# Kernel tuning notes

Hardware: AMD Instinct MI355X
Metric: run time of the kernel (lower is better)

The kernel has to match this reference:

```python
import jax, jax.numpy as jnp
import numpy as np

D_MODEL = 1024
N_LAYERS = 2
D_INNER = 2048   # expand_factor * d_model
D_STATE = 16
DT_RANK = 64     # ceil(d_model/16)
D_CONV = 4
BATCH = 2
SEQ = 1024
EPS = 1e-5


def setup_inputs() -> dict:
    key = jax.random.key(0)
    ks = jax.random.split(key, 8)
    s = 0.02
    x = jax.random.normal(ks[0], (BATCH, SEQ, D_MODEL), jnp.float32)
    norm_w = jnp.ones((N_LAYERS, D_MODEL), jnp.float32)
    in_proj_w = jax.random.normal(ks[1], (N_LAYERS, 2 * D_INNER, D_MODEL), jnp.float32) * s
    conv_w = jax.random.normal(ks[2], (N_LAYERS, D_INNER, D_CONV), jnp.float32) * s  # depthwise kernel
    conv_b = jnp.zeros((N_LAYERS, D_INNER), jnp.float32)
    x_proj_w = jax.random.normal(ks[3], (N_LAYERS, DT_RANK + 2 * D_STATE, D_INNER), jnp.float32) * s
    dt_std = DT_RANK ** -0.5
    dt_proj_w = jax.random.uniform(ks[4], (N_LAYERS, D_INNER, DT_RANK), jnp.float32, -dt_std, dt_std)
    dt = jnp.exp(jax.random.uniform(ks[5], (N_LAYERS, D_INNER), jnp.float32)
                 * (np.log(0.1) - np.log(0.001)) + np.log(0.001))
    dt = jnp.clip(dt, 1e-4)
    dt_proj_b = dt + jnp.log(-jnp.expm1(-dt))  # inverse softplus init
    A_log = jnp.broadcast_to(jnp.log(jnp.arange(1, D_STATE + 1, dtype=jnp.float32)),
                             (N_LAYERS, D_INNER, D_STATE)).copy()
    D_param = jnp.ones((N_LAYERS, D_INNER), jnp.float32)
    out_proj_w = jax.random.normal(ks[6], (N_LAYERS, D_MODEL, D_INNER), jnp.float32) * s
    return dict(x=x, norm_w=norm_w, in_proj_w=in_proj_w, conv_w=conv_w, conv_b=conv_b,
                x_proj_w=x_proj_w, dt_proj_w=dt_proj_w, dt_proj_b=dt_proj_b,
                A_log=A_log, D_param=D_param, out_proj_w=out_proj_w)


def _rms_norm(x, w):
    return x * jax.lax.rsqrt(jnp.mean(x * x, axis=-1, keepdims=True) + EPS) * w


def _silu(x):
    return x * jax.nn.sigmoid(x)


def _mamba_block(x, in_w, cw, cb, xp_w, dt_w, dt_b, A_log, Dp, out_w):
    # x: (B, L, D)
    xz = x @ in_w.T                      # (B, L, 2*ED)
    xc, z = jnp.split(xz, 2, axis=-1)    # each (B, L, ED)
    # causal depthwise conv1d (torch pads d_conv-1 both sides then slices [:L])
    xpad = jnp.pad(xc, ((0, 0), (D_CONV - 1, 0), (0, 0)))
    L = xc.shape[1]
    xc = sum(xpad[:, k:k + L, :] * cw[:, k] for k in range(D_CONV)) + cb
    xc = _silu(xc)
    # projections for delta, B, C
    dbc = xc @ xp_w.T                    # (B, L, dt_rank + 2N)
    delta = dbc[..., :DT_RANK]
    Bm = dbc[..., DT_RANK:DT_RANK + D_STATE]
    Cm = dbc[..., DT_RANK + D_STATE:]
    delta = jax.nn.softplus(delta @ dt_w.T + dt_b)      # (B, L, ED)
    A = -jnp.exp(A_log)                                 # (ED, N)
    dA = jnp.exp(delta[..., None] * A)                  # (B, L, ED, N)
    bx = (delta * xc)[..., None] * Bm[:, :, None, :]    # (B, L, ED, N)

    def combine(e1, e2):
        a1, b1 = e1
        a2, b2 = e2
        return a2 * a1, a2 * b1 + b2

    _, hs = jax.lax.associative_scan(combine, (dA, bx), axis=1)  # h_t = dA_t*h_{t-1} + bx_t
    y = jnp.einsum('blen,bln->ble', hs, Cm) + Dp * xc
    return (y * _silu(z)) @ out_w.T


def reference(x, norm_w, in_proj_w, conv_w, conv_b, x_proj_w, dt_proj_w, dt_proj_b,
              A_log, D_param, out_proj_w):
    for i in range(N_LAYERS):
        h = _rms_norm(x, norm_w[i])
        x = x + _mamba_block(h, in_proj_w[i], conv_w[i], conv_b[i], x_proj_w[i],
                             dt_proj_w[i], dt_proj_b[i], A_log[i], D_param[i], out_proj_w[i])
    return x
```

## Files before the change

kernel.cpp:

```cpp
#include <hip/hip_runtime.h>
#include <hip/hip_bf16.h>

#define BATCH   2
#define SEQ     1024
#define DMODEL  1024
#define DINNER  2048
#define DSTATE  16
#define DTRANK  64
#define DCONV   4
#define NLAYERS 2
#define ROWS    (BATCH*SEQ)
#define NCHUNK  32
#define CHUNK   32
#define KSPLIT  8
#define KSLICE  (DINNER / KSPLIT)
#define KSO     4
#define KSLICE_O (DINNER / KSO)

typedef unsigned short ushort_t;
typedef __attribute__((ext_vector_type(8))) short short8;
typedef __attribute__((ext_vector_type(4))) float f32x4;

__device__ __forceinline__ ushort_t f2bf(float f) {
  union { float f; unsigned u; } v; v.f = f;
  unsigned r = v.u + 0x7fffu + ((v.u >> 16) & 1u);
  return (ushort_t)(r >> 16);
}
__device__ __forceinline__ float bf2f(ushort_t h) {
  union { unsigned u; float f; } v; v.u = ((unsigned)h) << 16;
  return v.f;
}

__device__ __forceinline__ void g2lds16(const ushort_t* g, ushort_t* l) {
  __builtin_amdgcn_global_load_lds(
      (const __attribute__((address_space(1))) void*)g,
      (__attribute__((address_space(3))) void*)l, 16, 0, 0);
}

__device__ __forceinline__ void xcd_swz(int& bx, int& by) {
  const int nx = gridDim.x, nwg = nx * gridDim.y;
  int id = by * nx + bx;
  const int q = nwg >> 3;
  id = (id & 7) * q + (id >> 3);
  bx = id % nx; by = id / nx;
}

#define STG_Q(tid) (((tid) & 3) ^ (((tid) >> 3) & 3))
#define LDQ(lane)  ((((lane) >> 4) ^ (((lane) >> 1) & 3)) * 8)

__global__ __launch_bounds__(256) void cast_bf16_kernel(
    const float* __restrict__ in, ushort_t* __restrict__ out)
{
  const int i = blockIdx.x * 256 + threadIdx.x;
  const float4 v = reinterpret_cast<const float4*>(in)[i];
  ushort4 o;
  o.x = f2bf(v.x); o.y = f2bf(v.y); o.z = f2bf(v.z); o.w = f2bf(v.w);
  reinterpret_cast<ushort4*>(out)[i] = o;
}

__global__ __launch_bounds__(256) void init_rms_kernel(
    const float* __restrict__ x, const float* __restrict__ w,
    float* __restrict__ out, ushort_t* __restrict__ h16)
{
  const int row = blockIdx.x, t = threadIdx.x;
  const size_t base = (size_t)row * DMODEL + 4 * t;
  const float4 s = *reinterpret_cast<const float4*>(&x[base]);
  *reinterpret_cast<float4*>(&out[base]) = s;
  float ss = s.x * s.x + s.y * s.y + s.z * s.z + s.w * s.w;
  #pragma unroll
  for (int m = 1; m < 64; m <<= 1) ss += __shfl_xor(ss, m);
  __shared__ float red[4];
  if ((t & 63) == 0) red[t >> 6] = ss;
  __syncthreads();
  const float tot = red[0] + red[1] + red[2] + red[3];
  const float scale = rsqrtf(tot * (1.f / DMODEL) + 1e-5f);
  const float4 w4 = *reinterpret_cast<const float4*>(&w[4 * t]);
  ushort4 o;
  o.x = f2bf(s.x * scale * w4.x); o.y = f2bf(s.y * scale * w4.y);
  o.z = f2bf(s.z * scale * w4.z); o.w = f2bf(s.w * scale * w4.w);
  *reinterpret_cast<ushort4*>(&h16[base]) = o;
}

template<int MODE>
__global__ __launch_bounds__(256) void gemm_bf16_kernel(
    const ushort_t* __restrict__ A, const ushort_t* __restrict__ B,
    ushort_t* __restrict__ C2, const float* __restrict__ bias,
    int K, int lda, int ldb, int ldc)
{
  __shared__ __align__(16) ushort_t As[128 * 32];
  __shared__ __align__(16) ushort_t Bs[128 * 32];
  const int tid = threadIdx.x;
  const int lane = tid & 63, wid = tid >> 6;
  const int wr = wid >> 1, wc = wid & 1;
  int bx = blockIdx.x, by = blockIdx.y;
  xcd_swz(bx, by);
  const int row0 = by * 128, col0 = bx * 128;

  const int sq = STG_Q(tid) * 8;
  const ushort_t* ga0 = A + (size_t)(row0 + (tid >> 2)) * lda + sq;
  const ushort_t* ga1 = A + (size_t)(row0 + 64 + (tid >> 2)) * lda + sq;
  const ushort_t* gb0 = B + (size_t)(col0 + (tid >> 2)) * ldb + sq;
  const ushort_t* gb1 = B + (size_t)(col0 + 64 + (tid >> 2)) * ldb + sq;
  ushort_t* la0 = &As[tid * 8];
  ushort_t* la1 = &As[(256 + tid) * 8];
  ushort_t* lb0 = &Bs[tid * 8];
  ushort_t* lb1 = &Bs[(256 + tid) * 8];

  const int lk = LDQ(lane);
  const int lr16 = lane & 15;

  f32x4 acc[4][4] = {};

  for (int kb = 0; kb < K; kb += 32) {
    g2lds16(ga0 + kb, la0);
    g2lds16(ga1 + kb, la1);
    g2lds16(gb0 + kb, lb0);
    g2lds16(gb1 + kb, lb1);
    __syncthreads();

    short8 af[4], bfr[4];
    #pragma unroll
    for (int i = 0; i < 4; ++i)
      af[i] = *reinterpret_cast<const short8*>(
          &As[(wr * 64 + i * 16 + lr16) * 32 + lk]);
    #pragma unroll
    for (int j = 0; j < 4; ++j)
      bfr[j] = *reinterpret_cast<const short8*>(
          &Bs[(wc * 64 + j * 16 + lr16) * 32 + lk]);
    #pragma unroll
    for (int i = 0; i < 4; ++i)
      #pragma unroll
      for (int j = 0; j < 4; ++j)
        acc[i][j] = __builtin_amdgcn_mfma_f32_16x16x32_bf16(
            af[i], bfr[j], acc[i][j], 0, 0, 0);
    __syncthreads();
  }

  const int cr = (lane >> 4) * 4;
  #pragma unroll
  for (int i = 0; i < 4; ++i) {
    #pragma unroll
    for (int j = 0; j < 4; ++j) {
      const int col = col0 + wc * 64 + j * 16 + lr16;
      #pragma unroll
      for (int r = 0; r < 4; ++r) {
        const int row = row0 + wr * 64 + i * 16 + cr + r;
        float v = acc[i][j][r];
        if (MODE == 3) {
          v += bias[col];
          v = (v > 20.f) ? v : log1pf(__expf(v));
        }
        C2[(size_t)row * ldc + col] = f2bf(v);
      }
    }
  }
}

__global__ __launch_bounds__(256) void outproj_splitk_kernel(
    const ushort_t* __restrict__ A,
    const ushort_t* __restrict__ B,
    ushort_t* __restrict__ partial)
{
  __shared__ __align__(16) ushort_t As[128 * 32];
  __shared__ __align__(16) ushort_t Bs[128 * 32];
  const int tid = threadIdx.x;
  const int lane = tid & 63, wid = tid >> 6;
  const int wr = wid >> 1, wc = wid & 1;
  int bx = blockIdx.x, by = blockIdx.y;
  xcd_swz(bx, by);
  const int row0 = by * 128, col0 = bx * 128;
  const int k0 = blockIdx.z * KSLICE_O;

  const int sq = STG_Q(tid) * 8;
  const ushort_t* ga0 = A + (size_t)(row0 + (tid >> 2)) * DINNER + k0 + sq;
  const ushort_t* ga1 = A + (size_t)(row0 + 64 + (tid >> 2)) * DINNER + k0 + sq;
  const ushort_t* gb0 = B + (size_t)(col0 + (tid >> 2)) * DINNER + k0 + sq;
  const ushort_t* gb1 = B + (size_t)(col0 + 64 + (tid >> 2)) * DINNER + k0 + sq;
  ushort_t* la0 = &As[tid * 8];
  ushort_t* la1 = &As[(256 + tid) * 8];
  ushort_t* lb0 = &Bs[tid * 8];
  ushort_t* lb1 = &Bs[(256 + tid) * 8];

  const int lk = LDQ(lane);
  const int lr16 = lane & 15;

  f32x4 acc[4][4] = {};

  for (int kb = 0; kb < KSLICE_O; kb += 32) {
    g2lds16(ga0 + kb, la0);
    g2lds16(ga1 + kb, la1);
    g2lds16(gb0 + kb, lb0);
    g2lds16(gb1 + kb, lb1);
    __syncthreads();

    short8 af[4], bfr[4];
    #pragma unroll
    for (int i = 0; i < 4; ++i)
      af[i] = *reinterpret_cast<const short8*>(
          &As[(wr * 64 + i * 16 + lr16) * 32 + lk]);
    #pragma unroll
    for (int j = 0; j < 4; ++j)
      bfr[j] = *reinterpret_cast<const short8*>(
          &Bs[(wc * 64 + j * 16 + lr16) * 32 + lk]);
    #pragma unroll
    for (int i = 0; i < 4; ++i)
      #pragma unroll
      for (int j = 0; j < 4; ++j)
        acc[i][j] = __builtin_amdgcn_mfma_f32_16x16x32_bf16(
            af[i], bfr[j], acc[i][j], 0, 0, 0);
    __syncthreads();
  }

  ushort_t* Cz = partial + (size_t)blockIdx.z * ROWS * DMODEL;
  const int cr = (lane >> 4) * 4;
  #pragma unroll
  for (int i = 0; i < 4; ++i) {
    #pragma unroll
    for (int j = 0; j < 4; ++j) {
      const int col = col0 + wc * 64 + j * 16 + lr16;
      #pragma unroll
      for (int r = 0; r < 4; ++r) {
        const int row = row0 + wr * 64 + i * 16 + cr + r;
        Cz[(size_t)row * DMODEL + col] = f2bf(acc[i][j][r]);
      }
    }
  }
}

template<bool RMS>
__global__ __launch_bounds__(256) void outproj_reduce_rms_kernel(
    const ushort_t* __restrict__ partial, const float* __restrict__ nw,
    float* __restrict__ out, ushort_t* __restrict__ h16)
{
  const int row = blockIdx.x, t = threadIdx.x;
  const size_t base = (size_t)row * DMODEL + 4 * t;
  float4 s = *reinterpret_cast<float4*>(&out[base]);
  #pragma unroll
  for (int z = 0; z < KSO; ++z) {
    const ushort4 p = *reinterpret_cast<const ushort4*>(
        &partial[(size_t)z * ROWS * DMODEL + base]);
    s.x += bf2f(p.x); s.y += bf2f(p.y); s.z += bf2f(p.z); s.w += bf2f(p.w);
  }
  *reinterpret_cast<float4*>(&out[base]) = s;
  if (RMS) {
    float ss = s.x * s.x + s.y * s.y + s.z * s.z + s.w * s.w;
    #pragma unroll
    for (int m = 1; m < 64; m <<= 1) ss += __shfl_xor(ss, m);
    __shared__ float red[4];
    if ((t & 63) == 0) red[t >> 6] = ss;
    __syncthreads();
    const float tot = red[0] + red[1] + red[2] + red[3];
    const float scale = rsqrtf(tot * (1.f / DMODEL) + 1e-5f);
    const float4 w4 = *reinterpret_cast<const float4*>(&nw[4 * t]);
    ushort4 o;
    o.x = f2bf(s.x * scale * w4.x); o.y = f2bf(s.y * scale * w4.y);
    o.z = f2bf(s.z * scale * w4.z); o.w = f2bf(s.w * scale * w4.w);
    *reinterpret_cast<ushort4*>(&h16[base]) = o;
  }
}

__global__ __launch_bounds__(256) void xproj_mfma_kernel(
    const ushort_t* __restrict__ A,
    const ushort_t* __restrict__ B,
    ushort_t* __restrict__ partial)
{
  __shared__ __align__(16) ushort_t As[128 * 32];
  __shared__ __align__(16) ushort_t Bs[96 * 32];
  const int tid = threadIdx.x;
  const int lane = tid & 63, wid = tid >> 6;
  int bx = blockIdx.x, by = blockIdx.y;
  xcd_swz(bx, by);
  const int kz = bx, row0 = by * 128;
  const int k0 = kz * KSLICE;

  const int sq = STG_Q(tid) * 8;
  const ushort_t* ga0 = A + (size_t)(row0 + (tid >> 2)) * DINNER + k0 + sq;
  const ushort_t* ga1 = A + (size_t)(row0 + 64 + (tid >> 2)) * DINNER + k0 + sq;
  const ushort_t* gb0 = B + (size_t)(tid >> 2) * DINNER + k0 + sq;
  const ushort_t* gb1 = B + (size_t)(64 + (tid >> 2)) * DINNER + k0 + sq;
  ushort_t* la0 = &As[tid * 8];
  ushort_t* la1 = &As[(256 + tid) * 8];
  ushort_t* lb0 = &Bs[tid * 8];
  ushort_t* lb1 = &Bs[(256 + tid) * 8];

  const int lk = LDQ(lane);
  const int lr16 = lane & 15;

  f32x4 acc[2][6] = {};

  for (int kb = 0; kb < KSLICE; kb += 32) {
    g2lds16(ga0 + kb, la0);
    g2lds16(ga1 + kb, la1);
    g2lds16(gb0 + kb, lb0);
    if (tid < 128) g2lds16(gb1 + kb, lb1);
    __syncthreads();

    short8 af[2], bfr[6];
    #pragma unroll
    for (int i = 0; i < 2; ++i)
      af[i] = *reinterpret_cast<const short8*>(
          &As[(wid * 32 + i * 16 + lr16) * 32 + lk]);
    #pragma unroll
    for (int j = 0; j < 6; ++j)
      bfr[j] = *reinterpret_cast<const short8*>(
          &Bs[(j * 16 + lr16) * 32 + lk]);
    #pragma unroll
    for (int i = 0; i < 2; ++i)
      #pragma unroll
      for (int j = 0; j < 6; ++j)
        acc[i][j] = __builtin_amdgcn_mfma_f32_16x16x32_bf16(
            af[i], bfr[j], acc[i][j], 0, 0, 0);
    __syncthreads();
  }

  const int cr = (lane >> 4) * 4;
  #pragma unroll
  for (int i = 0; i < 2; ++i) {
    #pragma unroll
    for (int j = 0; j < 6; ++j) {
      const int col = j * 16 + lr16;
      #pragma unroll
      for (int r = 0; r < 4; ++r) {
        const int row = row0 + wid * 32 + i * 16 + cr + r;
        partial[((size_t)kz * ROWS + row) * 96 + col] = f2bf(acc[i][j][r]);
      }
    }
  }
}

__global__ __launch_bounds__(256) void xproj_reduce_kernel(
    const ushort_t* __restrict__ partial, float* __restrict__ dbcBC,
    ushort_t* __restrict__ dl16)
{
  const int idx = blockIdx.x * 256 + threadIdx.x;
  const int row = idx / 96, j = idx % 96;
  float s = 0.f;
  #pragma unroll
  for (int z = 0; z < KSPLIT; ++z)
    s += bf2f(partial[(size_t)z * ROWS * 96 + idx]);
  if (j < DTRANK) dl16[row * DTRANK + j] = f2bf(s);
  else            dbcBC[row * 32 + (j - DTRANK)] = s;
}

__global__ __launch_bounds__(256) void conv_silu_kernel(
    const ushort_t* __restrict__ xz16,
    const float* __restrict__ cw, const float* __restrict__ cb,
    ushort_t* __restrict__ xc16)
{
  const int idx = blockIdx.x * 256 + threadIdx.x;
  const int e0 = (idx * 8) % DINNER;
  const int bl = (idx * 8) / DINNER;
  const int l  = bl % SEQ;
  float acc[8];
  #pragma unroll
  for (int j = 0; j < 8; ++j) acc[j] = cb[e0 + j];
  float4 w4[8];
  #pragma unroll
  for (int j = 0; j < 8; ++j)
    w4[j] = *reinterpret_cast<const float4*>(&cw[(e0 + j) * DCONV]);
  #pragma unroll
  for (int k = 0; k < DCONV; ++k) {
    const int lk = l + k - (DCONV - 1);
    if (lk >= 0) {
      const short8 v = *reinterpret_cast<const short8*>(
          &xz16[(size_t)(bl + k - (DCONV - 1)) * (2 * DINNER) + e0]);
      #pragma unroll
      for (int j = 0; j < 8; ++j) {
        const float wv = (k == 0) ? w4[j].x : (k == 1) ? w4[j].y
                        : (k == 2) ? w4[j].z : w4[j].w;
        acc[j] += bf2f((ushort_t)v[j]) * wv;
      }
    }
  }
  short8 o;
  #pragma unroll
  for (int j = 0; j < 8; ++j) {
    const float v = acc[j] / (1.f + __expf(-acc[j]));
    o[j] = (short)f2bf(v);
  }
  *reinterpret_cast<short8*>(&xc16[(size_t)bl * DINNER + e0]) = o;
}

__global__ __launch_bounds__(256) void scan_chunk_kernel(
    const ushort_t* __restrict__ d16,
    const ushort_t* __restrict__ xc16,
    const float* __restrict__ dbcBC,
    const float* __restrict__ A_log,
    ushort_t* __restrict__ P16,
    ushort_t* __restrict__ H16)
{
  __shared__ float sB[CHUNK][16];
  const int bc = blockIdx.y;
  const int b = bc / NCHUNK, c = bc % NCHUNK;
  const int e = blockIdx.x * 256 + threadIdx.x;
  const size_t row32 = ((size_t)b * SEQ + c * CHUNK) * 32;
  #pragma unroll
  for (int p = 0; p < (CHUNK * 16) / 256; ++p) {
    const int idx = threadIdx.x + p * 256;
    sB[idx >> 4][idx & 15] = dbcBC[row32 + (idx >> 4) * 32 + (idx & 15)];
  }
  float Aen[16];
  #pragma unroll
  for (int q = 0; q < 4; ++q) {
    const float4 a4 = *reinterpret_cast<const float4*>(&A_log[(size_t)e * 16 + q * 4]);
    Aen[q * 4 + 0] = -__expf(a4.x);
    Aen[q * 4 + 1] = -__expf(a4.y);
    Aen[q * 4 + 2] = -__expf(a4.z);
    Aen[q * 4 + 3] = -__expf(a4.w);
  }
  __syncthreads();

  float h[16];
  #pragma unroll
  for (int n = 0; n < 16; ++n) h[n] = 0.f;
  float sd = 0.f;
  const size_t rowE = ((size_t)b * SEQ + c * CHUNK) * DINNER + e;
  float dv = bf2f(d16[rowE]), xv = bf2f(xc16[rowE]);
  for (int t = 0; t < CHUNK; ++t) {
    float dvn = 0.f, xvn = 0.f;
    if (t + 1 < CHUNK) {
      dvn = bf2f(d16[rowE + (size_t)(t + 1) * DINNER]);
      xvn = bf2f(xc16[rowE + (size_t)(t + 1) * DINNER]);
    }
    const float dxv = dv * xv;
    sd += dv;
    #pragma unroll
    for (int n = 0; n < 16; ++n) {
      const float dA = __expf(dv * Aen[n]);
      h[n] = dA * h[n] + dxv * sB[t][n];
    }
    dv = dvn; xv = xvn;
  }
  const size_t o = ((size_t)bc * DINNER + e) * 16;
  #pragma unroll
  for (int q = 0; q < 4; ++q) {
    ushort4 pv, hv;
    pv.x = f2bf(__expf(Aen[q * 4 + 0] * sd));
    pv.y = f2bf(__expf(Aen[q * 4 + 1] * sd));
    pv.z = f2bf(__expf(Aen[q * 4 + 2] * sd));
    pv.w = f2bf(__expf(Aen[q * 4 + 3] * sd));
    hv.x = f2bf(h[q * 4 + 0]); hv.y = f2bf(h[q * 4 + 1]);
    hv.z = f2bf(h[q * 4 + 2]); hv.w = f2bf(h[q * 4 + 3]);
    *reinterpret_cast<ushort4*>(&P16[o + q * 4]) = pv;
    *reinterpret_cast<ushort4*>(&H16[o + q * 4]) = hv;
  }
}

__global__ __launch_bounds__(256) void scan_combine_kernel(
    const ushort_t* __restrict__ P16, ushort_t* __restrict__ H16)
{
  const int idx = blockIdx.x * 256 + threadIdx.x;
  const int b = idx >> 15;
  const int en = idx & (DINNER * 16 - 1);
  const size_t base = (size_t)b * NCHUNK * DINNER * 16 + en;
  float H = 0.f;
  float P = bf2f(P16[base]), hf = bf2f(H16[base]);
  for (int c = 0; c < NCHUNK; ++c) {
    const size_t o = base + (size_t)c * DINNER * 16;
    float Pn = 0.f, hfn = 0.f;
    if (c + 1 < NCHUNK) {
      const size_t on = o + (size_t)DINNER * 16;
      Pn = bf2f(P16[on]); hfn = bf2f(H16[on]);
    }
    H16[o] = f2bf(H);
    H = P * H + hf;
    P = Pn; hf = hfn;
  }
}

__global__ __launch_bounds__(256) void scan_out_kernel(
    const ushort_t* __restrict__ d16,
    const ushort_t* __restrict__ xc16,
    const float* __restrict__ dbcBC,
    const ushort_t* __restrict__ xz16,
    const float* __restrict__ A_log,
    const float* __restrict__ Dp,
    const ushort_t* __restrict__ H16,
    ushort_t* __restrict__ yz16)
{
  __shared__ float sB[CHUNK][16];
  __shared__ float sC[CHUNK][16];
  const int bc = blockIdx.y;
  const int b = bc / NCHUNK, c = bc % NCHUNK;
  const int e = blockIdx.x * 256 + threadIdx.x;
  const size_t row32 = ((size_t)b * SEQ + c * CHUNK) * 32;
  #pragma unroll
  for (int p = 0; p < (CHUNK * 32) / 256; ++p) {
    const int idx = threadIdx.x + p * 256;
    const int t = idx >> 5, j = idx & 31;
    const float v = dbcBC[row32 + t * 32 + j];
    if (j < 16) sB[t][j] = v; else sC[t][j - 16] = v;
  }
  float Aen[16];
  #pragma unroll
  for (int q = 0; q < 4; ++q) {
    const float4 a4 = *reinterpret_cast<const float4*>(&A_log[(size_t)e * 16 + q * 4]);
    Aen[q * 4 + 0] = -__expf(a4.x);
    Aen[q * 4 + 1] = -__expf(a4.y);
    Aen[q * 4 + 2] = -__expf(a4.z);
    Aen[q * 4 + 3] = -__expf(a4.w);
  }
  float h[16];
  const size_t oh = ((size_t)bc * DINNER + e) * 16;
  #pragma unroll
  for (int q = 0; q < 4; ++q) {
    const ushort4 hv = *reinterpret_cast<const ushort4*>(&H16[oh + q * 4]);
    h[q * 4 + 0] = bf2f(hv.x); h[q * 4 + 1] = bf2f(hv.y);
    h[q * 4 + 2] = bf2f(hv.z); h[q * 4 + 3] = bf2f(hv.w);
  }
  const float dpe = Dp[e];
  __syncthreads();

  const size_t rowE = ((size_t)b * SEQ + c * CHUNK) * DINNER + e;
  const size_t rowZ = ((size_t)b * SEQ + c * CHUNK) * (2 * DINNER) + DINNER + e;
  float dv = bf2f(d16[rowE]), xv = bf2f(xc16[rowE]);
  float zv = bf2f(xz16[rowZ]);
  for (int t = 0; t < CHUNK; ++t) {
    float dvn = 0.f, xvn = 0.f, zvn = 0.f;
    if (t + 1 < CHUNK) {
      dvn = bf2f(d16[rowE + (size_t)(t + 1) * DINNER]);
      xvn = bf2f(xc16[rowE + (size_t)(t + 1) * DINNER]);
      zvn = bf2f(xz16[rowZ + (size_t)(t + 1) * (2 * DINNER)]);
    }
    const float dxv = dv * xv;
    float y = dpe * xv;
    #pragma unroll
    for (int n = 0; n < 16; ++n) {
      const float dA = __expf(dv * Aen[n]);
      h[n] = dA * h[n] + dxv * sB[t][n];
      y += h[n] * sC[t][n];
    }
    const float sz = zv / (1.f + __expf(-zv));
    yz16[rowE + (size_t)t * DINNER] = f2bf(y * sz);
    dv = dvn; xv = xvn; zv = zvn;
  }
}

extern "C" void kernel_launch(void* const* d_in, const int* in_sizes, int n_in,
                              void* d_out, int out_size, void* d_ws, size_t ws_size,
                              hipStream_t stream)
{
  const float* x         = (const float*)d_in[0];
  const float* norm_w    = (const float*)d_in[1];
  const float* in_proj_w = (const float*)d_in[2];
  const float* conv_w    = (const float*)d_in[3];
  const float* conv_b    = (const float*)d_in[4];
  const float* x_proj_w  = (const float*)d_in[5];
  const float* dt_proj_w = (const float*)d_in[6];
  const float* dt_proj_b = (const float*)d_in[7];
  const float* A_log     = (const float*)d_in[8];
  const float* D_param   = (const float*)d_in[9];
  const float* out_proj_w= (const float*)d_in[10];
  float* out = (float*)d_out;

  const size_t M = 1024 * 1024;
  float* ws = (float*)d_ws;
  ushort_t* w16i_all = (ushort_t*)ws;
  ushort_t* w16o_all = (ushort_t*)(ws + 4 * M);
  ushort_t* xpw16_all= (ushort_t*)(ws + 6 * M);
  ushort_t* dtw16_all= (ushort_t*)(ws + 6 * M + 196608);
  float* dbcBC    = ws + 6 * M + 327680;
  ushort_t* dl16  = (ushort_t*)(ws + 6 * M + 393216);
  ushort_t* xz16  = (ushort_t*)(ws + 6 * M + 524288);
  ushort_t* partO = xz16;
  ushort_t* xc16  = (ushort_t*)(ws + 10 * M + 524288);
  ushort_t* d16   = (ushort_t*)(ws + 12 * M + 524288);
  ushort_t* P16   = (ushort_t*)(ws + 14 * M + 524288);
  ushort_t* H16   = (ushort_t*)(ws + 15 * M + 524288);
  ushort_t* yz16  = (ushort_t*)(ws + 16 * M + 524288);
  ushort_t* h16   = (ushort_t*)(ws + 18 * M + 524288);
  ushort_t* partX = (ushort_t*)(ws + 19 * M + 524288);

  cast_bf16_kernel<<<NLAYERS * 2 * DINNER * DMODEL / 1024, 256, 0, stream>>>(
      in_proj_w, w16i_all);
  cast_bf16_kernel<<<NLAYERS * DMODEL * DINNER / 1024, 256, 0, stream>>>(
      out_proj_w, w16o_all);
  cast_bf16_kernel<<<NLAYERS * 96 * DINNER / 1024, 256, 0, stream>>>(
      x_proj_w, xpw16_all);
  cast_bf16_kernel<<<NLAYERS * DINNER * DTRANK / 1024, 256, 0, stream>>>(
      dt_proj_w, dtw16_all);

  init_rms_kernel<<<ROWS, 256, 0, stream>>>(x, norm_w, out, h16);

  for (int layer = 0; layer < NLAYERS; ++layer) {
    const float* cw  = conv_w     + (size_t)layer * DINNER * DCONV;
    const float* cb  = conv_b     + (size_t)layer * DINNER;
    const float* dtb = dt_proj_b  + (size_t)layer * DINNER;
    const float* Al  = A_log      + (size_t)layer * DINNER * DSTATE;
    const float* Dpp = D_param    + (size_t)layer * DINNER;
    const ushort_t* w16i  = w16i_all  + (size_t)layer * 2 * DINNER * DMODEL;
    const ushort_t* w16o  = w16o_all  + (size_t)layer * DMODEL * DINNER;
    const ushort_t* xpw16 = xpw16_all + (size_t)layer * 96 * DINNER;
    const ushort_t* dtw16 = dtw16_all + (size_t)layer * DINNER * DTRANK;

    gemm_bf16_kernel<2>
        <<<dim3(2 * DINNER / 128, ROWS / 128), 256, 0, stream>>>(
            h16, w16i, xz16, nullptr, DMODEL, DMODEL, DMODEL, 2 * DINNER);

    conv_silu_kernel<<<(size_t)ROWS * DINNER / 8 / 256, 256, 0, stream>>>(
        xz16, cw, cb, xc16);

    xproj_mfma_kernel<<<dim3(KSPLIT, ROWS / 128), 256, 0, stream>>>(
        xc16, xpw16, partX);
    xproj_reduce_kernel<<<ROWS * 96 / 256, 256, 0, stream>>>(
        partX, dbcBC, dl16);

    gemm_bf16_kernel<3>
        <<<dim3(DINNER / 128, ROWS / 128), 256, 0, stream>>>(
            dl16, dtw16, d16, dtb, DTRANK, DTRANK, DTRANK, DINNER);

    scan_chunk_kernel<<<dim3(DINNER / 256, BATCH * NCHUNK), 256, 0, stream>>>(
        d16, xc16, dbcBC, Al, P16, H16);
    scan_combine_kernel<<<BATCH * DINNER * 16 / 256, 256, 0, stream>>>(
        P16, H16);
    scan_out_kernel<<<dim3(DINNER / 256, BATCH * NCHUNK), 256, 0, stream>>>(
        d16, xc16, dbcBC, xz16, Al, Dpp, H16, yz16);

    outproj_splitk_kernel
        <<<dim3(DMODEL / 128, ROWS / 128, KSO), 256, 0, stream>>>(
            yz16, w16o, partO);

    if (layer + 1 < NLAYERS) {
      outproj_reduce_rms_kernel<true><<<ROWS, 256, 0, stream>>>(
          partO, norm_w + (size_t)(layer + 1) * DMODEL, out, h16);
    } else {
      outproj_reduce_rms_kernel<false><<<ROWS, 256, 0, stream>>>(
          partO, nullptr, out, nullptr);
    }
  }
}
```

Baseline: 315.2 us.

## Split-K the in-projection GEMM and sum partials inside conv and scan consumers

The in-projection GEMM now runs as a 2-way split-K GEMM that writes two bf16 partial slabs, doubling the grid from 512 to 1024 blocks. There is no separate reduce pass: the conv kernel and the scan output kernel read both slabs and add them on the fly. The out-projection split-K kernel is generalized into a shared template for both GEMMs. The scan kernels also fold log2(e) into A so they can use exp2f instead of __expf. The cost is twice the global read traffic for xz in the consumers, plus an extra bf16 rounding step on the partial sums.

After: 355.6 us. +12.8%, slower.

```diff
diff --git a/kernel.cpp b/kernel.cpp
--- a/kernel.cpp
+++ b/kernel.cpp
@@ -16,6 +16,9 @@
 #define KSLICE  (DINNER / KSPLIT)
 #define KSO     4
 #define KSLICE_O (DINNER / KSO)
+#define KSI     2
+#define KSLICE_I (DMODEL / KSI)
+#define LOG2E   1.44269504088896f
 
 typedef unsigned short ushort_t;
 typedef __attribute__((ext_vector_type(8))) short short8;
@@ -81,8 +84,7 @@
   *reinterpret_cast<ushort4*>(&h16[base]) = o;
 }
 
-template<int MODE>
-__global__ __launch_bounds__(256) void gemm_bf16_kernel(
+__global__ __launch_bounds__(256) void gemm_dtproj_kernel(
     const ushort_t* __restrict__ A, const ushort_t* __restrict__ B,
     ushort_t* __restrict__ C2, const float* __restrict__ bias,
     int K, int lda, int ldb, int ldc)
@@ -145,21 +147,18 @@
       #pragma unroll
       for (int r = 0; r < 4; ++r) {
         const int row = row0 + wr * 64 + i * 16 + cr + r;
-        float v = acc[i][j][r];
-        if (MODE == 3) {
-          v += bias[col];
-          v = (v > 20.f) ? v : log1pf(__expf(v));
-        }
+        float v = acc[i][j][r] + bias[col];
+        v = (v > 20.f) ? v : log1pf(__expf(v));
         C2[(size_t)row * ldc + col] = f2bf(v);
       }
     }
   }
 }
 
-__global__ __launch_bounds__(256) void outproj_splitk_kernel(
-    const ushort_t* __restrict__ A,
-    const ushort_t* __restrict__ B,
-    ushort_t* __restrict__ partial)
+template<int KS>
+__global__ __launch_bounds__(256) void splitk_gemm_kernel(
+    const ushort_t* __restrict__ A, const ushort_t* __restrict__ B,
+    ushort_t* __restrict__ partial, int ldk, int ldc)
 {
   __shared__ __align__(16) ushort_t As[128 * 32];
   __shared__ __align__(16) ushort_t Bs[128 * 32];
@@ -169,13 +168,13 @@
   int bx = blockIdx.x, by = blockIdx.y;
   xcd_swz(bx, by);
   const int row0 = by * 128, col0 = bx * 128;
-  const int k0 = blockIdx.z * KSLICE_O;
+  const int k0 = blockIdx.z * KS;
 
   const int sq = STG_Q(tid) * 8;
-  const ushort_t* ga0 = A + (size_t)(row0 + (tid >> 2)) * DINNER + k0 + sq;
-  const ushort_t* ga1 = A + (size_t)(row0 + 64 + (tid >> 2)) * DINNER + k0 + sq;
-  const ushort_t* gb0 = B + (size_t)(col0 + (tid >> 2)) * DINNER + k0 + sq;
-  const ushort_t* gb1 = B + (size_t)(col0 + 64 + (tid >> 2)) * DINNER + k0 + sq;
+  const ushort_t* ga0 = A + (size_t)(row0 + (tid >> 2)) * ldk + k0 + sq;
+  const ushort_t* ga1 = A + (size_t)(row0 + 64 + (tid >> 2)) * ldk + k0 + sq;
+  const ushort_t* gb0 = B + (size_t)(col0 + (tid >> 2)) * ldk + k0 + sq;
+  const ushort_t* gb1 = B + (size_t)(col0 + 64 + (tid >> 2)) * ldk + k0 + sq;
   ushort_t* la0 = &As[tid * 8];
   ushort_t* la1 = &As[(256 + tid) * 8];
   ushort_t* lb0 = &Bs[tid * 8];
@@ -186,7 +185,7 @@
 
   f32x4 acc[4][4] = {};
 
-  for (int kb = 0; kb < KSLICE_O; kb += 32) {
+  for (int kb = 0; kb < KS; kb += 32) {
     g2lds16(ga0 + kb, la0);
     g2lds16(ga1 + kb, la1);
     g2lds16(gb0 + kb, lb0);
@@ -211,7 +210,7 @@
     __syncthreads();
   }
 
-  ushort_t* Cz = partial + (size_t)blockIdx.z * ROWS * DMODEL;
+  ushort_t* Cz = partial + (size_t)blockIdx.z * ROWS * ldc;
   const int cr = (lane >> 4) * 4;
   #pragma unroll
   for (int i = 0; i < 4; ++i) {
@@ -221,7 +220,7 @@
       #pragma unroll
       for (int r = 0; r < 4; ++r) {
         const int row = row0 + wr * 64 + i * 16 + cr + r;
-        Cz[(size_t)row * DMODEL + col] = f2bf(acc[i][j][r]);
+        Cz[(size_t)row * ldc + col] = f2bf(acc[i][j][r]);
       }
     }
   }
@@ -343,10 +342,11 @@
 }
 
 __global__ __launch_bounds__(256) void conv_silu_kernel(
-    const ushort_t* __restrict__ xz16,
+    const ushort_t* __restrict__ pI,
     const float* __restrict__ cw, const float* __restrict__ cb,
     ushort_t* __restrict__ xc16)
 {
+  const size_t SLAB = (size_t)ROWS * 2 * DINNER;
   const int idx = blockIdx.x * 256 + threadIdx.x;
   const int e0 = (idx * 8) % DINNER;
   const int bl = (idx * 8) / DINNER;
@@ -362,13 +362,14 @@
   for (int k = 0; k < DCONV; ++k) {
     const int lk = l + k - (DCONV - 1);
     if (lk >= 0) {
-      const short8 v = *reinterpret_cast<const short8*>(
-          &xz16[(size_t)(bl + k - (DCONV - 1)) * (2 * DINNER) + e0]);
+      const size_t o = (size_t)(bl + k - (DCONV - 1)) * (2 * DINNER) + e0;
+      const short8 v0 = *reinterpret_cast<const short8*>(&pI[o]);
+      const short8 v1 = *reinterpret_cast<const short8*>(&pI[o + SLAB]);
       #pragma unroll
       for (int j = 0; j < 8; ++j) {
         const float wv = (k == 0) ? w4[j].x : (k == 1) ? w4[j].y
                         : (k == 2) ? w4[j].z : w4[j].w;
-        acc[j] += bf2f((ushort_t)v[j]) * wv;
+        acc[j] += (bf2f((ushort_t)v0[j]) + bf2f((ushort_t)v1[j])) * wv;
       }
     }
   }
@@ -403,10 +404,10 @@
   #pragma unroll
   for (int q = 0; q < 4; ++q) {
     const float4 a4 = *reinterpret_cast<const float4*>(&A_log[(size_t)e * 16 + q * 4]);
-    Aen[q * 4 + 0] = -__expf(a4.x);
-    Aen[q * 4 + 1] = -__expf(a4.y);
-    Aen[q * 4 + 2] = -__expf(a4.z);
-    Aen[q * 4 + 3] = -__expf(a4.w);
+    Aen[q * 4 + 0] = -__expf(a4.x) * LOG2E;
+    Aen[q * 4 + 1] = -__expf(a4.y) * LOG2E;
+    Aen[q * 4 + 2] = -__expf(a4.z) * LOG2E;
+    Aen[q * 4 + 3] = -__expf(a4.w) * LOG2E;
   }
   __syncthreads();
 
@@ -426,7 +427,7 @@
     sd += dv;
     #pragma unroll
     for (int n = 0; n < 16; ++n) {
-      const float dA = __expf(dv * Aen[n]);
+      const float dA = exp2f(dv * Aen[n]);
       h[n] = dA * h[n] + dxv * sB[t][n];
     }
     dv = dvn; xv = xvn;
@@ -435,10 +436,10 @@
   #pragma unroll
   for (int q = 0; q < 4; ++q) {
     ushort4 pv, hv;
-    pv.x = f2bf(__expf(Aen[q * 4 + 0] * sd));
-    pv.y = f2bf(__expf(Aen[q * 4 + 1] * sd));
-    pv.z = f2bf(__expf(Aen[q * 4 + 2] * sd));
-    pv.w = f2bf(__expf(Aen[q * 4 + 3] * sd));
+    pv.x = f2bf(exp2f(Aen[q * 4 + 0] * sd));
+    pv.y = f2bf(exp2f(Aen[q * 4 + 1] * sd));
+    pv.z = f2bf(exp2f(Aen[q * 4 + 2] * sd));
+    pv.w = f2bf(exp2f(Aen[q * 4 + 3] * sd));
     hv.x = f2bf(h[q * 4 + 0]); hv.y = f2bf(h[q * 4 + 1]);
     hv.z = f2bf(h[q * 4 + 2]); hv.w = f2bf(h[q * 4 + 3]);
     *reinterpret_cast<ushort4*>(&P16[o + q * 4]) = pv;
@@ -472,7 +473,7 @@
     const ushort_t* __restrict__ d16,
     const ushort_t* __restrict__ xc16,
     const float* __restrict__ dbcBC,
-    const ushort_t* __restrict__ xz16,
+    const ushort_t* __restrict__ pI,
     const float* __restrict__ A_log,
     const float* __restrict__ Dp,
     const ushort_t* __restrict__ H16,
@@ -480,6 +481,7 @@
 {
   __shared__ float sB[CHUNK][16];
   __shared__ float sC[CHUNK][16];
+  const size_t SLAB = (size_t)ROWS * 2 * DINNER;
   const int bc = blockIdx.y;
   const int b = bc / NCHUNK, c = bc % NCHUNK;
   const int e = blockIdx.x * 256 + threadIdx.x;
@@ -495,10 +497,10 @@
   #pragma unroll
   for (int q = 0; q < 4; ++q) {
     const float4 a4 = *reinterpret_cast<const float4*>(&A_log[(size_t)e * 16 + q * 4]);
-    Aen[q * 4 + 0] = -__expf(a4.x);
-    Aen[q * 4 + 1] = -__expf(a4.y);
-    Aen[q * 4 + 2] = -__expf(a4.z);
-    Aen[q * 4 + 3] = -__expf(a4.w);
+    Aen[q * 4 + 0] = -__expf(a4.x) * LOG2E;
+    Aen[q * 4 + 1] = -__expf(a4.y) * LOG2E;
+    Aen[q * 4 + 2] = -__expf(a4.z) * LOG2E;
+    Aen[q * 4 + 3] = -__expf(a4.w) * LOG2E;
   }
   float h[16];
   const size_t oh = ((size_t)bc * DINNER + e) * 16;
@@ -514,19 +516,20 @@
   const size_t rowE = ((size_t)b * SEQ + c * CHUNK) * DINNER + e;
   const size_t rowZ = ((size_t)b * SEQ + c * CHUNK) * (2 * DINNER) + DINNER + e;
   float dv = bf2f(d16[rowE]), xv = bf2f(xc16[rowE]);
-  float zv = bf2f(xz16[rowZ]);
+  float zv = bf2f(pI[rowZ]) + bf2f(pI[rowZ + SLAB]);
   for (int t = 0; t < CHUNK; ++t) {
     float dvn = 0.f, xvn = 0.f, zvn = 0.f;
     if (t + 1 < CHUNK) {
       dvn = bf2f(d16[rowE + (size_t)(t + 1) * DINNER]);
       xvn = bf2f(xc16[rowE + (size_t)(t + 1) * DINNER]);
-      zvn = bf2f(xz16[rowZ + (size_t)(t + 1) * (2 * DINNER)]);
+      const size_t zo = rowZ + (size_t)(t + 1) * (2 * DINNER);
+      zvn = bf2f(pI[zo]) + bf2f(pI[zo + SLAB]);
     }
     const float dxv = dv * xv;
     float y = dpe * xv;
     #pragma unroll
     for (int n = 0; n < 16; ++n) {
-      const float dA = __expf(dv * Aen[n]);
+      const float dA = exp2f(dv * Aen[n]);
       h[n] = dA * h[n] + dxv * sB[t][n];
       y += h[n] * sC[t][n];
     }
@@ -561,15 +564,15 @@
   ushort_t* dtw16_all= (ushort_t*)(ws + 6 * M + 196608);
   float* dbcBC    = ws + 6 * M + 327680;
   ushort_t* dl16  = (ushort_t*)(ws + 6 * M + 393216);
-  ushort_t* xz16  = (ushort_t*)(ws + 6 * M + 524288);
-  ushort_t* partO = xz16;
-  ushort_t* xc16  = (ushort_t*)(ws + 10 * M + 524288);
-  ushort_t* d16   = (ushort_t*)(ws + 12 * M + 524288);
-  ushort_t* P16   = (ushort_t*)(ws + 14 * M + 524288);
-  ushort_t* H16   = (ushort_t*)(ws + 15 * M + 524288);
-  ushort_t* yz16  = (ushort_t*)(ws + 16 * M + 524288);
-  ushort_t* h16   = (ushort_t*)(ws + 18 * M + 524288);
-  ushort_t* partX = (ushort_t*)(ws + 19 * M + 524288);
+  ushort_t* partI = (ushort_t*)(ws + 6 * M + 524288);
+  ushort_t* partO = partI;
+  ushort_t* xc16  = (ushort_t*)(ws + 14 * M + 524288);
+  ushort_t* d16   = (ushort_t*)(ws + 16 * M + 524288);
+  ushort_t* P16   = (ushort_t*)(ws + 18 * M + 524288);
+  ushort_t* H16   = (ushort_t*)(ws + 19 * M + 524288);
+  ushort_t* yz16  = (ushort_t*)(ws + 20 * M + 524288);
+  ushort_t* h16   = (ushort_t*)(ws + 22 * M + 524288);
+  ushort_t* partX = (ushort_t*)(ws + 23 * M + 524288);
 
   cast_bf16_kernel<<<NLAYERS * 2 * DINNER * DMODEL / 1024, 256, 0, stream>>>(
       in_proj_w, w16i_all);
@@ -593,19 +596,19 @@
     const ushort_t* xpw16 = xpw16_all + (size_t)layer * 96 * DINNER;
     const ushort_t* dtw16 = dtw16_all + (size_t)layer * DINNER * DTRANK;
 
-    gemm_bf16_kernel<2>
-        <<<dim3(2 * DINNER / 128, ROWS / 128), 256, 0, stream>>>(
-            h16, w16i, xz16, nullptr, DMODEL, DMODEL, DMODEL, 2 * DINNER);
+    splitk_gemm_kernel<KSLICE_I>
+        <<<dim3(2 * DINNER / 128, ROWS / 128, KSI), 256, 0, stream>>>(
+            h16, w16i, partI, DMODEL, 2 * DINNER);
 
     conv_silu_kernel<<<(size_t)ROWS * DINNER / 8 / 256, 256, 0, stream>>>(
-        xz16, cw, cb, xc16);
+        partI, cw, cb, xc16);
 
     xproj_mfma_kernel<<<dim3(KSPLIT, ROWS / 128), 256, 0, stream>>>(
         xc16, xpw16, partX);
     xproj_reduce_kernel<<<ROWS * 96 / 256, 256, 0, stream>>>(
         partX, dbcBC, dl16);
 
-    gemm_bf16_kernel<3>
+    gemm_dtproj_kernel
         <<<dim3(DINNER / 128, ROWS / 128), 256, 0, stream>>>(
             dl16, dtw16, d16, dtb, DTRANK, DTRANK, DTRANK, DINNER);
 
@@ -614,11 +617,11 @@
     scan_combine_kernel<<<BATCH * DINNER * 16 / 256, 256, 0, stream>>>(
         P16, H16);
     scan_out_kernel<<<dim3(DINNER / 256, BATCH * NCHUNK), 256, 0, stream>>>(
-        d16, xc16, dbcBC, xz16, Al, Dpp, H16, yz16);
-
-    outproj_splitk_kernel
+        d16, xc16, dbcBC, partI, Al, Dpp, H16, yz16);
+
+    splitk_gemm_kernel<KSLICE_O>
         <<<dim3(DMODEL / 128, ROWS / 128, KSO), 256, 0, stream>>>(
-            yz16, w16o, partO);
+            yz16, w16o, partO, DINNER, DMODEL);
 
     if (layer + 1 < NLAYERS) {
       outproj_reduce_rms_kernel<true><<<ROWS, 256, 0, stream>>>(
```
